# Performance work log

Measured on AMD Instinct MI355X. Metric: run time of the kernel, lower is better.

## Reference

```python
import jax, jax.numpy as jnp
import numpy as np

N_EMBED = 1024
HEAD_SIZE = 128
B, T = 4, 2048

def setup_inputs() -> dict:
    key = jax.random.key(0)
    kx, kq, kk, kv = jax.random.split(key, 4)
    bound = 1.0 / np.sqrt(N_EMBED)  # torch Linear default init range
    x = jax.random.normal(kx, (B, T, N_EMBED), dtype=jnp.float32)
    Wq = jax.random.uniform(kq, (N_EMBED, HEAD_SIZE), jnp.float32, -bound, bound)
    Wk = jax.random.uniform(kk, (N_EMBED, HEAD_SIZE), jnp.float32, -bound, bound)
    Wv = jax.random.uniform(kv, (N_EMBED, HEAD_SIZE), jnp.float32, -bound, bound)
    return {"x": x, "Wq": Wq, "Wk": Wk, "Wv": Wv}

def reference(x, Wq, Wk, Wv):
    Bn, Tn, C = x.shape
    q = x @ Wq  # [B,T,H]
    k = x @ Wk
    v = x @ Wv
    # NOTE: original scales by C**-0.5 where C = n_embed (not head_size)
    scale = C ** (-0.5)
    wei = jnp.einsum('bqh,bkh->bqk', q, k) * scale  # [B,T,T]
    causal = jnp.tril(jnp.ones((Tn, Tn), dtype=bool))
    wei = jnp.where(causal, wei, -jnp.inf)
    wei = jax.nn.softmax(wei, axis=-1)
    # dropout p=0.0 -> identity
    return jnp.einsum('bqk,bkh->bqh', wei, v)
```

## Files before the change

### kernel.cpp

```cpp
#include <hip/hip_runtime.h>
#include <stdint.h>

#define B_ 4
#define T_ 2048
#define C_ 1024
#define H_ 128
#define NEG_BIG -3.0e38f

typedef __attribute__((ext_vector_type(8))) short short8;
typedef __attribute__((ext_vector_type(4))) float f32x4;
typedef __attribute__((ext_vector_type(4))) unsigned short ushort4v;
typedef __attribute__((ext_vector_type(8))) unsigned short ushort8v;

__device__ __forceinline__ unsigned short f2bf(float f) {
  union { float f; unsigned u; } cv; cv.f = f;
  return (unsigned short)((cv.u + 0x8000u) >> 16);
}

__device__ __forceinline__ float bf2f(unsigned short s) {
  union { unsigned u; float f; } cv; cv.u = ((unsigned)s) << 16;
  return cv.f;
}

#define CSCALE 0.045084220027780106f

__global__ __launch_bounds__(256, 3) void qkv_proj(const float* __restrict__ x,
                                                   const float* __restrict__ Wq,
                                                   const float* __restrict__ Wk,
                                                   const float* __restrict__ Wv,
                                                   unsigned short* __restrict__ Qb,
                                                   unsigned short* __restrict__ Kb,
                                                   unsigned short* __restrict__ VT) {
  __shared__ unsigned short As[2][64 * 64];
  __shared__ unsigned short Bs[2][64 * 64];

  const int tid  = threadIdx.x;
  const int wave = tid >> 6, lane = tid & 63;
  const int quad = lane >> 4, l15 = lane & 15;
  const int rb = blockIdx.x & 127, cb = blockIdx.x >> 7;
  const int gm0 = rb * 64, gn0 = cb * 64;
  const int wm = wave >> 1, wn = wave & 1;

  const int bn = tid & 63, bkc = tid >> 6;
  const float* Wsrc = (cb < 2) ? Wq : (cb < 4) ? Wk : Wv;
  const int bh = (gn0 & 127) + bn;

  const int axr = tid >> 3, axc = tid & 7;
  const float* gAx = x + (size_t)(gm0 + axr) * C_ + axc * 8;

  int aoff[2][2], boff[2][2];
#pragma unroll
  for (int mt = 0; mt < 2; ++mt) {
    const int r = wm * 32 + mt * 16 + l15;
#pragma unroll
    for (int ks = 0; ks < 2; ++ks)
      aoff[mt][ks] = r * 64 + (((ks * 4 + quad) ^ r) & 7) * 8;
  }
#pragma unroll
  for (int nt = 0; nt < 2; ++nt) {
    const int r = wn * 32 + nt * 16 + l15;
#pragma unroll
    for (int ks = 0; ks < 2; ++ks)
      boff[nt][ks] = r * 64 + ((((ks * 4 + quad)) ^ r ^ (r >> 3)) & 7) * 8;
  }

  f32x4 acc[2][2];
  const f32x4 zero4 = {0.f, 0.f, 0.f, 0.f};
#pragma unroll
  for (int mt = 0; mt < 2; ++mt)
#pragma unroll
    for (int nt = 0; nt < 2; ++nt) acc[mt][nt] = zero4;

#define LOAD_B(ko_)                                                                \
  _Pragma("unroll")                                                                \
  for (int kk = 0; kk < 16; ++kk)                                                  \
    bv[kk] = Wsrc[(size_t)((ko_) + bkc * 16 + kk) * 128 + bh];

#define WRITE_B(buf)                                                               \
  {                                                                                \
    short8 bw0, bw1;                                                               \
    _Pragma("unroll")                                                              \
    for (int e = 0; e < 8; ++e) {                                                  \
      bw0[e] = (short)f2bf(bv[e]);                                                 \
      bw1[e] = (short)f2bf(bv[8 + e]);                                             \
    }                                                                              \
    const int sx = bn ^ (bn >> 3);                                                 \
    *(short8*)(&Bs[buf][bn * 64 + (((bkc * 2) ^ sx) & 7) * 8]) = bw0;              \
    *(short8*)(&Bs[buf][bn * 64 + (((bkc * 2 + 1) ^ sx) & 7) * 8]) = bw1;          \
  }

#define LOAD_A(ko_)                                                                \
  _Pragma("unroll")                                                                \
  for (int q = 0; q < 2; ++q) {                                                    \
    av0[q] = *(const f32x4*)(gAx + (size_t)(q * 32) * C_ + (ko_));                 \
    av1[q] = *(const f32x4*)(gAx + (size_t)(q * 32) * C_ + (ko_) + 4);             \
  }

#define WRITE_A(buf)                                                               \
  _Pragma("unroll")                                                                \
  for (int q = 0; q < 2; ++q) {                                                    \
    const int row = axr + q * 32;                                                  \
    short8 aw;                                                                     \
    _Pragma("unroll")                                                              \
    for (int e = 0; e < 4; ++e) {                                                  \
      aw[e]     = (short)f2bf(av0[q][e]);                                          \
      aw[4 + e] = (short)f2bf(av1[q][e]);                                          \
    }                                                                              \
    *(short8*)(&As[buf][row * 64 + ((axc ^ row) & 7) * 8]) = aw;                   \
  }

  f32x4 av0[2], av1[2];
  float bv[16];
  LOAD_A(0);
  LOAD_B(0);
  WRITE_A(0);
  WRITE_B(0);

  for (int kb = 0; kb < 16; ++kb) {
    __syncthreads();
    const int cur = kb & 1, nxt = cur ^ 1;
    if (kb + 1 < 16) {
      LOAD_A((kb + 1) * 64);
      LOAD_B((kb + 1) * 64);
    }
    const unsigned short* Ac = As[cur];
    const unsigned short* Bc = Bs[cur];
#pragma unroll
    for (int ks = 0; ks < 2; ++ks) {
      short8 b0 = *(const short8*)(Bc + boff[0][ks]);
      short8 b1 = *(const short8*)(Bc + boff[1][ks]);
#pragma unroll
      for (int mt = 0; mt < 2; ++mt) {
        short8 a = *(const short8*)(Ac + aoff[mt][ks]);
        acc[mt][0] = __builtin_amdgcn_mfma_f32_16x16x32_bf16(a, b0, acc[mt][0], 0, 0, 0);
        acc[mt][1] = __builtin_amdgcn_mfma_f32_16x16x32_bf16(a, b1, acc[mt][1], 0, 0, 0);
      }
    }
    if (kb + 1 < 16) {
      WRITE_A(nxt);
      WRITE_B(nxt);
    }
  }
#undef LOAD_B
#undef WRITE_B
#undef LOAD_A
#undef WRITE_A

#pragma unroll
  for (int mt = 0; mt < 2; ++mt) {
    const int row0 = gm0 + wm * 32 + mt * 16 + quad * 4;
#pragma unroll
    for (int nt = 0; nt < 2; ++nt) {
      const int colbase = gn0 + wn * 32 + nt * 16;
      const int col = colbase + l15;
      if (colbase < 128) {
#pragma unroll
        for (int r = 0; r < 4; ++r)
          Qb[(size_t)(row0 + r) * H_ + col] = f2bf(acc[mt][nt][r] * CSCALE);
      } else if (colbase < 256) {
#pragma unroll
        for (int r = 0; r < 4; ++r)
          Kb[(size_t)(row0 + r) * H_ + (col - 128)] = f2bf(acc[mt][nt][r]);
      } else {
        const int h = col - 256;
        const int bidx = row0 >> 11;
        const int t0 = row0 & 2047;
        ushort4v pk;
        pk[0] = f2bf(acc[mt][nt][0]); pk[1] = f2bf(acc[mt][nt][1]);
        pk[2] = f2bf(acc[mt][nt][2]); pk[3] = f2bf(acc[mt][nt][3]);
        *(ushort4v*)(VT + (size_t)(bidx * H_ + h) * T_ + t0) = pk;
      }
    }
  }
}

__global__ __launch_bounds__(256, 3) void attn1(const unsigned short* __restrict__ Qb,
                                                const unsigned short* __restrict__ Kb,
                                                const unsigned short* __restrict__ VT,
                                                unsigned short* __restrict__ Opart,
                                                float* __restrict__ mpart,
                                                float* __restrict__ lpart) {
  __shared__ unsigned short Ks[64 * 128];
  __shared__ unsigned short Vs[128 * 64];
  __shared__ unsigned short Pls[4][16 * 72];

  const int bid = blockIdx.x;
  const int b  = bid & 3;
  const int jp = (bid >> 2) & 15;
  const int ch = bid >> 6;
  const int j1 = jp, j2 = 31 - jp;
  const int n1 = (ch <= j1) ? (((j1 - ch) >> 3) + 1) : 0;
  const int n2 = ((j2 - ch) >> 3) + 1;
  const int ntt = n1 + n2;

  const int tid  = threadIdx.x;
  const int wave = tid >> 6, lane = tid & 63;
  const int quad = lane >> 4, l15 = lane & 15;

  const unsigned short* Kb_b = Kb + (size_t)(b * T_) * H_;
  const unsigned short* VT_b = VT + (size_t)(b * H_) * T_;

  const int k_row4 = lane >> 4, k_slot = lane & 15;
  const int v_row8 = lane >> 3, v_slot = lane & 7;

  f32x4 kreg[4], vreg[4];

#define TILE(i_) (((i_) < n1) ? (ch + ((i_) << 3)) : (ch + (((i_) - n1) << 3)))

#define LOAD_KV(kv0_)                                                              \
  {                                                                                \
    _Pragma("unroll")                                                              \
    for (int i_ = 0; i_ < 4; ++i_) {                                               \
      const int r = wave * 16 + i_ * 4 + k_row4;                                   \
      const int c2 = (k_slot & 8) | ((k_slot ^ r) & 7);                            \
      kreg[i_] = *(const f32x4*)(Kb_b + (size_t)((kv0_) + r) * H_ + c2 * 8);       \
    }                                                                              \
    _Pragma("unroll")                                                              \
    for (int i_ = 0; i_ < 4; ++i_) {                                               \
      const int h = wave * 32 + i_ * 8 + v_row8;                                   \
      vreg[i_] = *(const f32x4*)(VT_b + (size_t)h * T_ + (kv0_) + ((v_slot ^ h) & 7) * 8); \
    }                                                                              \
  }

#define WRITE_KV()                                                                 \
  {                                                                                \
    _Pragma("unroll")                                                              \
    for (int i_ = 0; i_ < 4; ++i_) {                                               \
      const int r = wave * 16 + i_ * 4 + k_row4;                                   \
      *(f32x4*)(&Ks[r * 128 + k_slot * 8]) = kreg[i_];                             \
    }                                                                              \
    _Pragma("unroll")                                                              \
    for (int i_ = 0; i_ < 4; ++i_) {                                               \
      const int h = wave * 32 + i_ * 8 + v_row8;                                   \
      *(f32x4*)(&Vs[h * 64 + v_slot * 8]) = vreg[i_];                              \
    }                                                                              \
  }

#define EPI(jr_)                                                                   \
  {                                                                                \
    const int pid = (b * 32 + (jr_)) * 8 + ch;                                     \
    unsigned short* po = Opart + (size_t)(pid * 64 + wave * 16) * H_;              \
    _Pragma("unroll")                                                              \
    for (int nth = 0; nth < 8; ++nth)                                              \
      _Pragma("unroll")                                                            \
      for (int r = 0; r < 4; ++r)                                                  \
        po[(quad * 4 + r) * H_ + nth * 16 + l15] = f2bf(O[nth][r]);                \
    if (lane < 16) {                                                               \
      mpart[pid * 64 + wave * 16 + lane] = m_;                                     \
      lpart[pid * 64 + wave * 16 + lane] = l_;                                     \
    }                                                                              \
  }

  int jr_cur = n1 ? j1 : j2;
  short8 aq[4];
  {
    const unsigned short* qrow = Qb + (size_t)(b * T_ + jr_cur * 64 + wave * 16 + l15) * H_;
#pragma unroll
    for (int ks = 0; ks < 4; ++ks)
      aq[ks] = *(const short8*)(qrow + ks * 32 + quad * 8);
  }

  LOAD_KV(TILE(0) * 64);
  WRITE_KV();
  LOAD_KV(TILE(1) * 64);
  __syncthreads();

  const f32x4 zero4 = {0.f, 0.f, 0.f, 0.f};
  f32x4 O[8];
#pragma unroll
  for (int nth = 0; nth < 8; ++nth) O[nth] = zero4;
  float m_ = NEG_BIG, l_ = 0.f;

  for (int i = 0; i < ntt; ++i) {
    if (n1 && i == n1) {
      EPI(j1);
      m_ = NEG_BIG; l_ = 0.f;
#pragma unroll
      for (int nth = 0; nth < 8; ++nth) O[nth] = zero4;
      jr_cur = j2;
      const unsigned short* qrow = Qb + (size_t)(b * T_ + j2 * 64 + wave * 16 + l15) * H_;
#pragma unroll
      for (int ks = 0; ks < 4; ++ks)
        aq[ks] = *(const short8*)(qrow + ks * 32 + quad * 8);
    }
    const int ti  = TILE(i);
    const int kv0 = ti * 64;

    f32x4 ST[4];
    ST[0] = zero4; ST[1] = zero4; ST[2] = zero4; ST[3] = zero4;
    __builtin_amdgcn_s_setprio(1);
#pragma unroll
    for (int ntl = 0; ntl < 4; ++ntl) {
      const int kvr = ntl * 16 + l15;
#pragma unroll
      for (int ks = 0; ks < 4; ++ks) {
        const int c = ks * 4 + quad;
        const int slot = (c & 8) | ((c ^ kvr) & 7);
        short8 kf = *(const short8*)(Ks + kvr * 128 + slot * 8);
        ST[ntl] = __builtin_amdgcn_mfma_f32_16x16x32_bf16(kf, aq[ks], ST[ntl], 0, 0, 0);
      }
    }
    __builtin_amdgcn_s_setprio(0);

    if (ti == jr_cur) {
      const int ql = jr_cur * 64 + wave * 16 + l15;
#pragma unroll
      for (int ntl = 0; ntl < 4; ++ntl)
#pragma unroll
        for (int r = 0; r < 4; ++r) {
          const int kl = kv0 + ntl * 16 + quad * 4 + r;
          if (kl > ql) ST[ntl][r] = NEG_BIG;
        }
    }

    float pmax = ST[0][0];
#pragma unroll
    for (int ntl = 0; ntl < 4; ++ntl)
#pragma unroll
      for (int r = 0; r < 4; ++r) pmax = fmaxf(pmax, ST[ntl][r]);
    pmax = fmaxf(pmax, __shfl_xor(pmax, 16));
    pmax = fmaxf(pmax, __shfl_xor(pmax, 32));
    if (!__all(pmax <= m_ + 8.f)) {
      const float mn = fmaxf(m_, pmax);
      const float alpha = __builtin_amdgcn_exp2f(m_ - mn);
      m_ = mn;
      l_ *= alpha;
      float alr[4];
#pragma unroll
      for (int r = 0; r < 4; ++r) alr[r] = __shfl(alpha, quad * 4 + r);
#pragma unroll
      for (int nth = 0; nth < 8; ++nth)
#pragma unroll
        for (int r = 0; r < 4; ++r) O[nth][r] *= alr[r];
    }
    float s = 0.f;
#pragma unroll
    for (int ntl = 0; ntl < 4; ++ntl)
#pragma unroll
      for (int r = 0; r < 4; ++r) {
        const float p = __builtin_amdgcn_exp2f(ST[ntl][r] - m_);
        ST[ntl][r] = p;
        s += p;
      }
    s += __shfl_xor(s, 16);
    s += __shfl_xor(s, 32);
    l_ += s;

#pragma unroll
    for (int ntl = 0; ntl < 4; ++ntl) {
      ushort4v pk;
      pk[0] = f2bf(ST[ntl][0]); pk[1] = f2bf(ST[ntl][1]);
      pk[2] = f2bf(ST[ntl][2]); pk[3] = f2bf(ST[ntl][3]);
      *(ushort4v*)(&Pls[wave][l15 * 72 + ntl * 16 + quad * 4]) = pk;
    }

    short8 ap0 = *(const short8*)(&Pls[wave][l15 * 72 + quad * 8]);
    short8 ap1 = *(const short8*)(&Pls[wave][l15 * 72 + 32 + quad * 8]);
    __builtin_amdgcn_s_setprio(1);
#pragma unroll
    for (int nth = 0; nth < 8; ++nth) {
      const int h = nth * 16 + l15;
      short8 v0 = *(const short8*)(Vs + h * 64 + ((quad ^ h) & 7) * 8);
      short8 v1 = *(const short8*)(Vs + h * 64 + (((4 + quad) ^ h) & 7) * 8);
      O[nth] = __builtin_amdgcn_mfma_f32_16x16x32_bf16(ap0, v0, O[nth], 0, 0, 0);
      O[nth] = __builtin_amdgcn_mfma_f32_16x16x32_bf16(ap1, v1, O[nth], 0, 0, 0);
    }
    __builtin_amdgcn_s_setprio(0);

    if (i + 1 < ntt) {
      __syncthreads();
      WRITE_KV();
      if (i + 2 < ntt) LOAD_KV(TILE(i + 2) * 64);
      __syncthreads();
    }
  }
  EPI(j2);
#undef TILE
#undef LOAD_KV
#undef WRITE_KV
#undef EPI
}

__global__ __launch_bounds__(256) void attn2(const unsigned short* __restrict__ Opart,
                                             const float* __restrict__ mpart,
                                             const float* __restrict__ lpart,
                                             float* __restrict__ out) {
  const int b = blockIdx.x & 3;
  const int j = (blockIdx.x >> 2) & 31;
  const int qi = blockIdx.x >> 7;
  const int nch = min(j + 1, 8);
  const int tid = threadIdx.x;
  const int q = (tid >> 4) + qi * 16;
  const int h0 = (tid & 15) * 8;
  const int pbase = (b * 32 + j) * 8;

  float m_fin = NEG_BIG;
  for (int ch = 0; ch < nch; ++ch)
    m_fin = fmaxf(m_fin, mpart[(pbase + ch) * 64 + q]);
  float lf = 0.f;
  float o[8];
#pragma unroll
  for (int c = 0; c < 8; ++c) o[c] = 0.f;
  for (int ch = 0; ch < nch; ++ch) {
    const int pid = pbase + ch;
    const float sc = __builtin_amdgcn_exp2f(mpart[pid * 64 + q] - m_fin);
    lf += sc * lpart[pid * 64 + q];
    ushort8v pv = *(const ushort8v*)(Opart + (size_t)(pid * 64 + q) * H_ + h0);
#pragma unroll
    for (int c = 0; c < 8; ++c) o[c] += sc * bf2f(pv[c]);
  }
  const float inv = 1.0f / lf;
  float* op = out + (size_t)(b * T_ + j * 64 + q) * H_ + h0;
  f32x4 v0 = {o[0] * inv, o[1] * inv, o[2] * inv, o[3] * inv};
  f32x4 v1 = {o[4] * inv, o[5] * inv, o[6] * inv, o[7] * inv};
  *(f32x4*)(op) = v0;
  *(f32x4*)(op + 4) = v1;
}

extern "C" void kernel_launch(void* const* d_in, const int* in_sizes, int n_in,
                              void* d_out, int out_size, void* d_ws, size_t ws_size,
                              hipStream_t stream) {
  const float* x  = (const float*)d_in[0];
  const float* Wq = (const float*)d_in[1];
  const float* Wk = (const float*)d_in[2];
  const float* Wv = (const float*)d_in[3];
  float* out = (float*)d_out;

  char* ws = (char*)d_ws;
  unsigned short* Qb  = (unsigned short*)(ws + 1048576);
  unsigned short* Kb  = (unsigned short*)(ws + 3145728);
  unsigned short* VT  = (unsigned short*)(ws + 5242880);
  unsigned short* Opart = (unsigned short*)(ws + 8388608);
  float* mpart = (float*)(ws + 25165824);
  float* lpart = (float*)(ws + 25427968);

  qkv_proj<<<dim3(768), dim3(256), 0, stream>>>(x, Wq, Wk, Wv, Qb, Kb, VT);
  attn1<<<dim3(512), dim3(256), 0, stream>>>(Qb, Kb, VT, Opart, mpart, lpart);
  attn2<<<dim3(512), dim3(256), 0, stream>>>(Opart, mpart, lpart, out);
}
```

Baseline: 115.3 us.

## Share each K/V tile between both paired query blocks in attn1

Each block handles two query blocks, j1 and j2, that read overlapping KV tiles. Before, it streamed the tiles for j1 and then again for j2. Now it walks the KV tiles once and applies each loaded tile to both query blocks, with two accumulator sets (O1/m1/l1 and O2/m2/l2). This roughly halves KV global loads and LDS writes, and cuts the number of barriers. The cost is doubled accumulator registers, so occupancy is lowered from 3 to 2 blocks per CU in launch_bounds.

Result: no change. 115.5 us (median of 3 runs) (+0.2%).

```diff
diff --git a/kernel.cpp b/kernel.cpp
--- a/kernel.cpp
+++ b/kernel.cpp
@@ -174,7 +174,7 @@
   }
 }
 
-__global__ __launch_bounds__(256, 3) void attn1(const unsigned short* __restrict__ Qb,
+__global__ __launch_bounds__(256, 2) void attn1(const unsigned short* __restrict__ Qb,
                                                 const unsigned short* __restrict__ Kb,
                                                 const unsigned short* __restrict__ VT,
                                                 unsigned short* __restrict__ Opart,
@@ -191,7 +191,6 @@
   const int j1 = jp, j2 = 31 - jp;
   const int n1 = (ch <= j1) ? (((j1 - ch) >> 3) + 1) : 0;
   const int n2 = ((j2 - ch) >> 3) + 1;
-  const int ntt = n1 + n2;
 
   const int tid  = threadIdx.x;
   const int wave = tid >> 6, lane = tid & 63;
@@ -204,8 +203,6 @@
   const int v_row8 = lane >> 3, v_slot = lane & 7;
 
   f32x4 kreg[4], vreg[4];
-
-#define TILE(i_) (((i_) < n1) ? (ch + ((i_) << 3)) : (ch + (((i_) - n1) << 3)))
 
 #define LOAD_KV(kv0_)                                                              \
   {                                                                                \
@@ -236,7 +233,87 @@
     }                                                                              \
   }
 
-#define EPI(jr_)                                                                   \
+#define PROCESS(jr_, aq_, O_, mv_, lv_)                                            \
+  {                                                                                \
+    f32x4 ST[4];                                                                   \
+    ST[0] = zero4; ST[1] = zero4; ST[2] = zero4; ST[3] = zero4;                    \
+    __builtin_amdgcn_s_setprio(1);                                                 \
+    _Pragma("unroll")                                                              \
+    for (int ntl = 0; ntl < 4; ++ntl) {                                            \
+      const int kvr = ntl * 16 + l15;                                              \
+      _Pragma("unroll")                                                            \
+      for (int ks = 0; ks < 4; ++ks) {                                             \
+        const int c = ks * 4 + quad;                                               \
+        const int slot = (c & 8) | ((c ^ kvr) & 7);                                \
+        short8 kf = *(const short8*)(Ks + kvr * 128 + slot * 8);                   \
+        ST[ntl] = __builtin_amdgcn_mfma_f32_16x16x32_bf16(kf, aq_[ks], ST[ntl], 0, 0, 0); \
+      }                                                                            \
+    }                                                                              \
+    __builtin_amdgcn_s_setprio(0);                                                 \
+    if (ti == (jr_)) {                                                             \
+      const int ql = (jr_) * 64 + wave * 16 + l15;                                 \
+      _Pragma("unroll")                                                            \
+      for (int ntl = 0; ntl < 4; ++ntl)                                            \
+        _Pragma("unroll")                                                          \
+        for (int r = 0; r < 4; ++r) {                                              \
+          const int kl = kv0 + ntl * 16 + quad * 4 + r;                            \
+          if (kl > ql) ST[ntl][r] = NEG_BIG;                                       \
+        }                                                                          \
+    }                                                                              \
+    float pmax = ST[0][0];                                                         \
+    _Pragma("unroll")                                                              \
+    for (int ntl = 0; ntl < 4; ++ntl)                                              \
+      _Pragma("unroll")                                                            \
+      for (int r = 0; r < 4; ++r) pmax = fmaxf(pmax, ST[ntl][r]);                  \
+    pmax = fmaxf(pmax, __shfl_xor(pmax, 16));                                      \
+    pmax = fmaxf(pmax, __shfl_xor(pmax, 32));                                      \
+    if (!__all(pmax <= (mv_) + 8.f)) {                                             \
+      const float mn = fmaxf((mv_), pmax);                                         \
+      const float alpha = __builtin_amdgcn_exp2f((mv_) - mn);                      \
+      (mv_) = mn;                                                                  \
+      (lv_) *= alpha;                                                              \
+      float alr[4];                                                                \
+      _Pragma("unroll")                                                            \
+      for (int r = 0; r < 4; ++r) alr[r] = __shfl(alpha, quad * 4 + r);            \
+      _Pragma("unroll")                                                            \
+      for (int nth = 0; nth < 8; ++nth)                                            \
+        _Pragma("unroll")                                                          \
+        for (int r = 0; r < 4; ++r) O_[nth][r] *= alr[r];                          \
+    }                                                                              \
+    float s = 0.f;                                                                 \
+    _Pragma("unroll")                                                              \
+    for (int ntl = 0; ntl < 4; ++ntl)                                              \
+      _Pragma("unroll")                                                            \
+      for (int r = 0; r < 4; ++r) {                                                \
+        const float p = __builtin_amdgcn_exp2f(ST[ntl][r] - (mv_));                \
+        ST[ntl][r] = p;                                                            \
+        s += p;                                                                    \
+      }                                                                            \
+    s += __shfl_xor(s, 16);                                                        \
+    s += __shfl_xor(s, 32);                                                        \
+    (lv_) += s;                                                                    \
+    _Pragma("unroll")                                                              \
+    for (int ntl = 0; ntl < 4; ++ntl) {                                            \
+      ushort4v pk;                                                                 \
+      pk[0] = f2bf(ST[ntl][0]); pk[1] = f2bf(ST[ntl][1]);                          \
+      pk[2] = f2bf(ST[ntl][2]); pk[3] = f2bf(ST[ntl][3]);                          \
+      *(ushort4v*)(&Pls[wave][l15 * 72 + ntl * 16 + quad * 4]) = pk;               \
+    }                                                                              \
+    short8 ap0 = *(const short8*)(&Pls[wave][l15 * 72 + quad * 8]);                \
+    short8 ap1 = *(const short8*)(&Pls[wave][l15 * 72 + 32 + quad * 8]);           \
+    __builtin_amdgcn_s_setprio(1);                                                 \
+    _Pragma("unroll")                                                              \
+    for (int nth = 0; nth < 8; ++nth) {                                            \
+      const int h = nth * 16 + l15;                                                \
+      short8 v0 = *(const short8*)(Vs + h * 64 + ((quad ^ h) & 7) * 8);            \
+      short8 v1 = *(const short8*)(Vs + h * 64 + (((4 + quad) ^ h) & 7) * 8);      \
+      O_[nth] = __builtin_amdgcn_mfma_f32_16x16x32_bf16(ap0, v0, O_[nth], 0, 0, 0); \
+      O_[nth] = __builtin_amdgcn_mfma_f32_16x16x32_bf16(ap1, v1, O_[nth], 0, 0, 0); \
+    }                                                                              \
+    __builtin_amdgcn_s_setprio(0);                                                 \
+  }
+
+#define EPI(jr_, O_, mv_, lv_)                                                     \
   {                                                                                \
     const int pid = (b * 32 + (jr_)) * 8 + ch;                                     \
     unsigned short* po = Opart + (size_t)(pid * 64 + wave * 16) * H_;              \
@@ -244,140 +321,57 @@
     for (int nth = 0; nth < 8; ++nth)                                              \
       _Pragma("unroll")                                                            \
       for (int r = 0; r < 4; ++r)                                                  \
-        po[(quad * 4 + r) * H_ + nth * 16 + l15] = f2bf(O[nth][r]);                \
+        po[(quad * 4 + r) * H_ + nth * 16 + l15] = f2bf(O_[nth][r]);               \
     if (lane < 16) {                                                               \
-      mpart[pid * 64 + wave * 16 + lane] = m_;                                     \
-      lpart[pid * 64 + wave * 16 + lane] = l_;                                     \
-    }                                                                              \
-  }
-
-  int jr_cur = n1 ? j1 : j2;
-  short8 aq[4];
+      mpart[pid * 64 + wave * 16 + lane] = (mv_);                                  \
+      lpart[pid * 64 + wave * 16 + lane] = (lv_);                                  \
+    }                                                                              \
+  }
+
+  short8 aq1[4], aq2[4];
   {
-    const unsigned short* qrow = Qb + (size_t)(b * T_ + jr_cur * 64 + wave * 16 + l15) * H_;
+    const unsigned short* q2row = Qb + (size_t)(b * T_ + j2 * 64 + wave * 16 + l15) * H_;
 #pragma unroll
     for (int ks = 0; ks < 4; ++ks)
-      aq[ks] = *(const short8*)(qrow + ks * 32 + quad * 8);
-  }
-
-  LOAD_KV(TILE(0) * 64);
+      aq2[ks] = *(const short8*)(q2row + ks * 32 + quad * 8);
+  }
+  if (n1) {
+    const unsigned short* q1row = Qb + (size_t)(b * T_ + j1 * 64 + wave * 16 + l15) * H_;
+#pragma unroll
+    for (int ks = 0; ks < 4; ++ks)
+      aq1[ks] = *(const short8*)(q1row + ks * 32 + quad * 8);
+  }
+
+  LOAD_KV(ch * 64);
   WRITE_KV();
-  LOAD_KV(TILE(1) * 64);
+  if (n2 > 1) LOAD_KV((ch + 8) * 64);
   __syncthreads();
 
   const f32x4 zero4 = {0.f, 0.f, 0.f, 0.f};
-  f32x4 O[8];
-#pragma unroll
-  for (int nth = 0; nth < 8; ++nth) O[nth] = zero4;
-  float m_ = NEG_BIG, l_ = 0.f;
-
-  for (int i = 0; i < ntt; ++i) {
-    if (n1 && i == n1) {
-      EPI(j1);
-      m_ = NEG_BIG; l_ = 0.f;
-#pragma unroll
-      for (int nth = 0; nth < 8; ++nth) O[nth] = zero4;
-      jr_cur = j2;
-      const unsigned short* qrow = Qb + (size_t)(b * T_ + j2 * 64 + wave * 16 + l15) * H_;
-#pragma unroll
-      for (int ks = 0; ks < 4; ++ks)
-        aq[ks] = *(const short8*)(qrow + ks * 32 + quad * 8);
-    }
-    const int ti  = TILE(i);
+  f32x4 O1[8], O2[8];
+#pragma unroll
+  for (int nth = 0; nth < 8; ++nth) { O1[nth] = zero4; O2[nth] = zero4; }
+  float m1 = NEG_BIG, l1 = 0.f, m2 = NEG_BIG, l2 = 0.f;
+
+  for (int i = 0; i < n2; ++i) {
+    const int ti  = ch + (i << 3);
     const int kv0 = ti * 64;
 
-    f32x4 ST[4];
-    ST[0] = zero4; ST[1] = zero4; ST[2] = zero4; ST[3] = zero4;
-    __builtin_amdgcn_s_setprio(1);
-#pragma unroll
-    for (int ntl = 0; ntl < 4; ++ntl) {
-      const int kvr = ntl * 16 + l15;
-#pragma unroll
-      for (int ks = 0; ks < 4; ++ks) {
-        const int c = ks * 4 + quad;
-        const int slot = (c & 8) | ((c ^ kvr) & 7);
-        short8 kf = *(const short8*)(Ks + kvr * 128 + slot * 8);
-        ST[ntl] = __builtin_amdgcn_mfma_f32_16x16x32_bf16(kf, aq[ks], ST[ntl], 0, 0, 0);
-      }
-    }
-    __builtin_amdgcn_s_setprio(0);
-
-    if (ti == jr_cur) {
-      const int ql = jr_cur * 64 + wave * 16 + l15;
-#pragma unroll
-      for (int ntl = 0; ntl < 4; ++ntl)
-#pragma unroll
-        for (int r = 0; r < 4; ++r) {
-          const int kl = kv0 + ntl * 16 + quad * 4 + r;
-          if (kl > ql) ST[ntl][r] = NEG_BIG;
-        }
-    }
-
-    float pmax = ST[0][0];
-#pragma unroll
-    for (int ntl = 0; ntl < 4; ++ntl)
-#pragma unroll
-      for (int r = 0; r < 4; ++r) pmax = fmaxf(pmax, ST[ntl][r]);
-    pmax = fmaxf(pmax, __shfl_xor(pmax, 16));
-    pmax = fmaxf(pmax, __shfl_xor(pmax, 32));
-    if (!__all(pmax <= m_ + 8.f)) {
-      const float mn = fmaxf(m_, pmax);
-      const float alpha = __builtin_amdgcn_exp2f(m_ - mn);
-      m_ = mn;
-      l_ *= alpha;
-      float alr[4];
-#pragma unroll
-      for (int r = 0; r < 4; ++r) alr[r] = __shfl(alpha, quad * 4 + r);
-#pragma unroll
-      for (int nth = 0; nth < 8; ++nth)
-#pragma unroll
-        for (int r = 0; r < 4; ++r) O[nth][r] *= alr[r];
-    }
-    float s = 0.f;
-#pragma unroll
-    for (int ntl = 0; ntl < 4; ++ntl)
-#pragma unroll
-      for (int r = 0; r < 4; ++r) {
-        const float p = __builtin_amdgcn_exp2f(ST[ntl][r] - m_);
-        ST[ntl][r] = p;
-        s += p;
-      }
-    s += __shfl_xor(s, 16);
-    s += __shfl_xor(s, 32);
-    l_ += s;
-
-#pragma unroll
-    for (int ntl = 0; ntl < 4; ++ntl) {
-      ushort4v pk;
-      pk[0] = f2bf(ST[ntl][0]); pk[1] = f2bf(ST[ntl][1]);
-      pk[2] = f2bf(ST[ntl][2]); pk[3] = f2bf(ST[ntl][3]);
-      *(ushort4v*)(&Pls[wave][l15 * 72 + ntl * 16 + quad * 4]) = pk;
-    }
-
-    short8 ap0 = *(const short8*)(&Pls[wave][l15 * 72 + quad * 8]);
-    short8 ap1 = *(const short8*)(&Pls[wave][l15 * 72 + 32 + quad * 8]);
-    __builtin_amdgcn_s_setprio(1);
-#pragma unroll
-    for (int nth = 0; nth < 8; ++nth) {
-      const int h = nth * 16 + l15;
-      short8 v0 = *(const short8*)(Vs + h * 64 + ((quad ^ h) & 7) * 8);
-      short8 v1 = *(const short8*)(Vs + h * 64 + (((4 + quad) ^ h) & 7) * 8);
-      O[nth] = __builtin_amdgcn_mfma_f32_16x16x32_bf16(ap0, v0, O[nth], 0, 0, 0);
-      O[nth] = __builtin_amdgcn_mfma_f32_16x16x32_bf16(ap1, v1, O[nth], 0, 0, 0);
-    }
-    __builtin_amdgcn_s_setprio(0);
-
-    if (i + 1 < ntt) {
+    if (i < n1) PROCESS(j1, aq1, O1, m1, l1);
+    PROCESS(j2, aq2, O2, m2, l2);
+
+    if (i + 1 < n2) {
       __syncthreads();
       WRITE_KV();
-      if (i + 2 < ntt) LOAD_KV(TILE(i + 2) * 64);
+      if (i + 2 < n2) LOAD_KV((ch + ((i + 2) << 3)) * 64);
       __syncthreads();
     }
   }
-  EPI(j2);
-#undef TILE
+  if (n1) EPI(j1, O1, m1, l1);
+  EPI(j2, O2, m2, l2);
 #undef LOAD_KV
 #undef WRITE_KV
+#undef PROCESS
 #undef EPI
 }
 
```
